# Performance work log

Hardware: AMD Instinct MI355X
Metric: run time of the kernel (lower is better)

## Reference

```python
import jax, jax.numpy as jnp
import numpy as np

DELTA_A, DELTA_R = 0.1, 1.0
ALPHA, BETA, GAMMA = 1.0, 1.0, 0.001


def setup_inputs() -> dict:
    key = jax.random.key(0)
    B, D, H, W, K = 4, 32, 512, 512, 16
    out = jax.random.normal(key, (B, D, H, W), dtype=jnp.float32)
    # 4x4 block partition -> K=16 instance labels, one center per block
    gh, gw = 4, 4
    bh, bw = H // gh, W // gw
    rows = np.arange(H) // bh  # [H]
    cols = np.arange(W) // bw  # [W]
    labels = (rows[:, None] * gw + cols[None, :]).astype(np.int32)  # [H,W]
    target = jnp.asarray(np.broadcast_to(labels, (B, H, W)).copy())
    ctr = np.array([[r * bh + bh // 2, c * bw + bw // 2]
                    for r in range(gh) for c in range(gw)], dtype=np.int32)  # [K,2]
    centers = jnp.asarray(np.broadcast_to(ctr, (B, K, 2)).copy())
    return {"out": out, "target": target, "centers": centers, "batch_size": B}


def _safe_sqrt(x):
    # matches torch.linalg.norm subgradient 0 at 0 (avoids NaN grads)
    pos = x > 0
    return jnp.where(pos, jnp.sqrt(jnp.where(pos, x, 1.0)), 0.0)


def _pairwise_norm(a, b):
    # a [M,D], b [N,D] -> [M,N] euclidean distances via gram trick
    d2 = (jnp.sum(a * a, 1)[:, None] + jnp.sum(b * b, 1)[None, :]
          - 2.0 * a @ b.T)
    return _safe_sqrt(jax.nn.relu(d2))


def _per_image(o, t, c):
    # o [D,H,W], t [H,W] int, c [K,2] int
    D = o.shape[0]
    K = c.shape[0]
    x = o.reshape(D, -1).T                      # [HW, D]
    E = o[:, c[:, 0], c[:, 1]].T                # [K, D] center embeddings
    lab_c = t[c[:, 0], c[:, 1]]                 # [K]
    mask = (t.reshape(-1)[None, :] == lab_c[:, None])  # [K, HW]
    # attraction: hinged distance of every cluster pixel to its center
    norms = _pairwise_norm(E, x)                # [K, HW]
    hinged = jax.nn.relu(norms - DELTA_A) * mask
    cnt = jnp.sum(mask, axis=1)
    denom = jnp.maximum(cnt - 1, 1).astype(o.dtype)
    s_att = jnp.sum(jnp.sum(hinged, axis=1) / denom)
    # repelling: pairwise center distances; diagonal contributes relu(delta_r)
    # per row and the original subtracts delta_r per center -> excluded
    nE = _pairwise_norm(E, E)                   # [K, K]
    s_rep = jnp.sum(jax.nn.relu(DELTA_R - nE)) - K * DELTA_R
    # regularization: norm of each center embedding
    s_reg = jnp.sum(_safe_sqrt(jnp.sum(E * E, axis=1)))
    return s_att, s_rep, s_reg


def reference(out, target, centers, batch_size):
    K = centers.shape[1]
    s_att, s_rep, s_reg = jax.vmap(_per_image)(out, target, centers)  # [B] each
    div_att = jnp.float32(K)
    div_rep = jnp.float32(K * (K - 1))
    div_reg = jnp.float32(K)

    def step(carry, s):
        a, r, g = carry
        sa, sr, sg = s
        return ((a + sa) / div_att, (r + sr) / div_rep, (g + sg) / div_reg), None

    zero = jnp.float32(0.0)
    (att, rep, reg), _ = jax.lax.scan(step, (zero, zero, zero),
                                      (s_att, s_rep, s_reg))
    loss = ALPHA * att + BETA * rep + GAMMA * reg
    return loss, att, rep
```

## Files before the change

### kernel.cpp

```cpp
#include <hip/hip_runtime.h>
#include <hip/hip_bf16.h>

#define B_ 4
#define D_ 32
#define H_ 512
#define W_ 512
#define K_ 16
#define N_ (H_ * W_)
#define NQ_ (N_ / 4)
#define NBLK_ 256
#define EPAD 33

#define WS_SUM  0
#define WS_CNT  64
#define WS_E2   128
#define WS_LAB  192
#define WS_E    264
#define WS_PART 4096

typedef float vfloat4 __attribute__((ext_vector_type(4)));
typedef int vint4 __attribute__((ext_vector_type(4)));

__device__ inline vfloat4 nt_load_f4(const float* p) {
  return __builtin_nontemporal_load((const vfloat4*)p);
}
__device__ inline vint4 nt_load_i4(const int* p) {
  return __builtin_nontemporal_load((const vint4*)p);
}

__global__ __launch_bounds__(64) void setup_kernel(
    const float* __restrict__ outp, const int* __restrict__ target,
    const int* __restrict__ centers, float* __restrict__ ws) {
  const int b = blockIdx.x, k = blockIdx.y;
  const int lane = threadIdx.x;
  const int cy = centers[(b * K_ + k) * 2 + 0];
  const int cx = centers[(b * K_ + k) * 2 + 1];
  float v = 0.0f;
  if (lane < D_) {
    v = outp[(((size_t)b * D_ + lane) * H_ + cy) * W_ + cx];
    ws[WS_E + (b * K_ + k) * D_ + lane] = v;
  }
  float s = v * v;
  for (int off = 32; off > 0; off >>= 1) s += __shfl_xor(s, off, 64);
  if (lane == 0) {
    ws[WS_E2 + b * K_ + k] = s;
    ((int*)ws)[WS_LAB + b * K_ + k] = target[(size_t)b * N_ + cy * W_ + cx];
  }
}

__global__ __launch_bounds__(256) void attract_kernel(
    const float* __restrict__ outp, const int* __restrict__ target,
    float* __restrict__ ws) {
  const int b = blockIdx.y;
  const int tid = threadIdx.x;
  __shared__ float sE[K_ * EPAD];
  __shared__ float se2[K_];
  __shared__ int slab[K_];
  __shared__ float bs[K_];
  __shared__ float bc[K_];

  if (tid < 128) {
    const vfloat4 v = *(const vfloat4*)(ws + WS_E + b * (K_ * D_) + tid * 4);
    const int k = tid >> 3, d = (tid & 7) * 4;
    sE[k * EPAD + d + 0] = v.x;
    sE[k * EPAD + d + 1] = v.y;
    sE[k * EPAD + d + 2] = v.z;
    sE[k * EPAD + d + 3] = v.w;
  }
  if (tid < K_) {
    se2[tid] = ws[WS_E2 + b * K_ + tid];
    slab[tid] = ((const int*)ws)[WS_LAB + b * K_ + tid];
    bs[tid] = 0.0f;
    bc[tid] = 0.0f;
  }
  __syncthreads();

  const int q = blockIdx.x * 256 + tid;
  const float* xb = outp + (size_t)b * D_ * N_;
  const vint4 lab4 = nt_load_i4(target + (size_t)b * N_ + 4 * q);
  const int labv[4] = {lab4.x, lab4.y, lab4.z, lab4.w};

  int kf[4], nm[4];
#pragma unroll
  for (int j = 0; j < 4; ++j) { kf[j] = 0; nm[j] = 0; }
#pragma unroll
  for (int k = 0; k < K_; ++k) {
    const int lk = slab[k];
#pragma unroll
    for (int j = 0; j < 4; ++j) {
      if (labv[j] == lk) { if (nm[j] == 0) kf[j] = k; nm[j]++; }
    }
  }

  float dot[4] = {0.f, 0.f, 0.f, 0.f};
  float x2[4] = {0.f, 0.f, 0.f, 0.f};
#pragma unroll
  for (int d = 0; d < D_; ++d) {
    const vfloat4 x = nt_load_f4(xb + (size_t)d * N_ + 4 * q);
    const float xs[4] = {x.x, x.y, x.z, x.w};
#pragma unroll
    for (int j = 0; j < 4; ++j) {
      const float e = sE[kf[j] * EPAD + d];
      dot[j] = fmaf(xs[j], e, dot[j]);
      x2[j] = fmaf(xs[j], xs[j], x2[j]);
    }
  }

  float hv[4];
#pragma unroll
  for (int j = 0; j < 4; ++j) {
    const float d2 = x2[j] + se2[kf[j]] - 2.0f * dot[j];
    const float h = fmaxf(sqrtf(fmaxf(d2, 0.0f)) - 0.1f, 0.0f);
    hv[j] = (nm[j] > 0) ? h : 0.0f;
  }
  const bool same = (kf[0] == kf[1]) & (kf[1] == kf[2]) & (kf[2] == kf[3]);
  if (same) {
    const float cs = (float)((nm[0] > 0) + (nm[1] > 0) + (nm[2] > 0) + (nm[3] > 0));
    if (cs > 0.0f) {
      atomicAdd(&bs[kf[0]], hv[0] + hv[1] + hv[2] + hv[3]);
      atomicAdd(&bc[kf[0]], cs);
    }
  } else {
#pragma unroll
    for (int j = 0; j < 4; ++j) {
      if (nm[j] > 0) {
        atomicAdd(&bs[kf[j]], hv[j]);
        atomicAdd(&bc[kf[j]], 1.0f);
      }
    }
  }

  const bool extra = (nm[0] > 1) | (nm[1] > 1) | (nm[2] > 1) | (nm[3] > 1);
  if (__any(extra)) {
    for (int k = 0; k < K_; ++k) {
      bool need[4]; bool anyn = false;
#pragma unroll
      for (int j = 0; j < 4; ++j) {
        need[j] = (nm[j] > 1) && (labv[j] == slab[k]) && (k != kf[j]);
        anyn |= need[j];
      }
      if (__any(anyn)) {
        float dt[4] = {0.f, 0.f, 0.f, 0.f};
        for (int d = 0; d < D_; ++d) {
          const vfloat4 x = nt_load_f4(xb + (size_t)d * N_ + 4 * q);
          const float e = sE[k * EPAD + d];
          dt[0] = fmaf(x.x, e, dt[0]);
          dt[1] = fmaf(x.y, e, dt[1]);
          dt[2] = fmaf(x.z, e, dt[2]);
          dt[3] = fmaf(x.w, e, dt[3]);
        }
#pragma unroll
        for (int j = 0; j < 4; ++j) {
          if (need[j]) {
            const float d2 = x2[j] + se2[k] - 2.0f * dt[j];
            atomicAdd(&bs[k], fmaxf(sqrtf(fmaxf(d2, 0.0f)) - 0.1f, 0.0f));
            atomicAdd(&bc[k], 1.0f);
          }
        }
      }
    }
  }
  __syncthreads();

  if (tid < 2 * K_) {
    float* p = ws + WS_PART + ((size_t)b * NBLK_ + blockIdx.x) * (2 * K_);
    p[tid] = (tid < K_) ? bs[tid] : bc[tid - K_];
  }
}

__global__ __launch_bounds__(256) void reduce_kernel(const float* __restrict__ ws_in,
                                                     float* __restrict__ ws) {
  const int b = blockIdx.x >> 4, k = blockIdx.x & 15;
  const int tid = threadIdx.x;
  const float* base = ws_in + WS_PART + (size_t)b * NBLK_ * (2 * K_);
  float s = 0.0f, c = 0.0f;
  for (int i = tid; i < NBLK_; i += 256) {
    s += base[i * (2 * K_) + k];
    c += base[i * (2 * K_) + K_ + k];
  }
  for (int off = 32; off > 0; off >>= 1) {
    s += __shfl_xor(s, off, 64);
    c += __shfl_xor(c, off, 64);
  }
  __shared__ float rs[4], rc[4];
  if ((tid & 63) == 0) { rs[tid >> 6] = s; rc[tid >> 6] = c; }
  __syncthreads();
  if (tid == 0) {
    ws[WS_SUM + b * K_ + k] = rs[0] + rs[1] + rs[2] + rs[3];
    ws[WS_CNT + b * K_ + k] = rc[0] + rc[1] + rc[2] + rc[3];
  }
}

__global__ __launch_bounds__(256) void final_kernel(const float* __restrict__ ws,
                                                    float* __restrict__ out) {
  __shared__ float sE[B_ * K_ * D_];
  __shared__ float sred[256];
  __shared__ float srep[B_];
  __shared__ float sreg[B_];
  __shared__ float ssa[B_];
  const int tid = threadIdx.x;
  for (int i = tid; i < B_ * K_ * D_; i += 256) sE[i] = ws[WS_E + i];
  __syncthreads();

  const int i = tid >> 4, j = tid & 15;
  for (int b = 0; b < B_; ++b) {
    float dotv = 0.0f;
#pragma unroll 8
    for (int d = 0; d < D_; ++d)
      dotv = fmaf(sE[(b * K_ + i) * D_ + d], sE[(b * K_ + j) * D_ + d], dotv);
    const float d2 = ws[WS_E2 + b * K_ + i] + ws[WS_E2 + b * K_ + j] - 2.0f * dotv;
    sred[tid] = fmaxf(1.0f - sqrtf(fmaxf(d2, 0.0f)), 0.0f);
    __syncthreads();
    for (int s = 128; s > 0; s >>= 1) {
      if (tid < s) sred[tid] += sred[tid + s];
      __syncthreads();
    }
    if (tid == 0) srep[b] = sred[0] - (float)K_;
    __syncthreads();
  }

  sred[tid] = (tid < B_ * K_) ? sqrtf(fmaxf(ws[WS_E2 + tid], 0.0f)) : 0.0f;
  __syncthreads();
  if (tid < B_) {
    float s = 0.0f;
    for (int k = 0; k < K_; ++k) s += sred[tid * K_ + k];
    sreg[tid] = s;
  }

  if (tid < B_ * K_) {
    const float c = ws[WS_CNT + tid];
    float v = ws[WS_SUM + tid] / fmaxf(c - 1.0f, 1.0f);
    for (int off = 1; off < K_; off <<= 1) v += __shfl_xor(v, off, 64);
    if ((tid & 15) == 0) ssa[tid >> 4] = v;
  }
  __syncthreads();

  if (tid == 0) {
    float att = 0.0f, rep = 0.0f, reg = 0.0f;
    for (int b = 0; b < B_; ++b) {
      att = (att + ssa[b]) / (float)K_;
      rep = (rep + srep[b]) / (float)(K_ * (K_ - 1));
      reg = (reg + sreg[b]) / (float)K_;
    }
    out[0] = att + rep + 0.001f * reg;
    out[1] = att;
    out[2] = rep;
  }
}

extern "C" void kernel_launch(void* const* d_in, const int* in_sizes, int n_in,
                              void* d_out, int out_size, void* d_ws, size_t ws_size,
                              hipStream_t stream) {
  const float* outp = (const float*)d_in[0];
  const int* target = (const int*)d_in[1];
  const int* centers = (const int*)d_in[2];
  float* ws = (float*)d_ws;
  float* out = (float*)d_out;

  setup_kernel<<<dim3(B_, K_), 64, 0, stream>>>(outp, target, centers, ws);
  attract_kernel<<<dim3(NBLK_, B_), 256, 0, stream>>>(outp, target, ws);
  reduce_kernel<<<dim3(B_ * K_), 256, 0, stream>>>(ws, ws);
  final_kernel<<<1, 256, 0, stream>>>(ws, out);
}
```

Measured before the change: 200.5 us.

## Fuse setup and reduce kernels into attract/final and add wave-level atomic aggregation

Each attract block now gathers the center embeddings, their squared norms and labels itself, which removes the separate setup launch at the cost of redundant center loads per block. The per-block partial reduction moves into the final kernel, so the dedicated reduce launch is gone. A 32-lane shuffle reduction collapses the shared-memory atomics when all lanes map to the same cluster. Together these cut the pipeline from four launches to two and reduce atomic contention.

Result: no change. 201.6 us (+0.6%).

```diff
diff --git a/kernel.cpp b/kernel.cpp
--- a/kernel.cpp
+++ b/kernel.cpp
@@ -1,5 +1,4 @@
 #include <hip/hip_runtime.h>
-#include <hip/hip_bf16.h>
 
 #define B_ 4
 #define D_ 32
@@ -28,50 +27,44 @@
   return __builtin_nontemporal_load((const vint4*)p);
 }
 
-__global__ __launch_bounds__(64) void setup_kernel(
+__global__ __launch_bounds__(256) void attract_kernel(
     const float* __restrict__ outp, const int* __restrict__ target,
     const int* __restrict__ centers, float* __restrict__ ws) {
-  const int b = blockIdx.x, k = blockIdx.y;
-  const int lane = threadIdx.x;
-  const int cy = centers[(b * K_ + k) * 2 + 0];
-  const int cx = centers[(b * K_ + k) * 2 + 1];
-  float v = 0.0f;
-  if (lane < D_) {
-    v = outp[(((size_t)b * D_ + lane) * H_ + cy) * W_ + cx];
-    ws[WS_E + (b * K_ + k) * D_ + lane] = v;
-  }
-  float s = v * v;
-  for (int off = 32; off > 0; off >>= 1) s += __shfl_xor(s, off, 64);
-  if (lane == 0) {
-    ws[WS_E2 + b * K_ + k] = s;
-    ((int*)ws)[WS_LAB + b * K_ + k] = target[(size_t)b * N_ + cy * W_ + cx];
-  }
-}
-
-__global__ __launch_bounds__(256) void attract_kernel(
-    const float* __restrict__ outp, const int* __restrict__ target,
-    float* __restrict__ ws) {
   const int b = blockIdx.y;
   const int tid = threadIdx.x;
   __shared__ float sE[K_ * EPAD];
   __shared__ float se2[K_];
   __shared__ int slab[K_];
+  __shared__ int scy[K_], scx[K_];
   __shared__ float bs[K_];
   __shared__ float bc[K_];
 
-  if (tid < 128) {
-    const vfloat4 v = *(const vfloat4*)(ws + WS_E + b * (K_ * D_) + tid * 4);
-    const int k = tid >> 3, d = (tid & 7) * 4;
-    sE[k * EPAD + d + 0] = v.x;
-    sE[k * EPAD + d + 1] = v.y;
-    sE[k * EPAD + d + 2] = v.z;
-    sE[k * EPAD + d + 3] = v.w;
-  }
-  if (tid < K_) {
-    se2[tid] = ws[WS_E2 + b * K_ + tid];
-    slab[tid] = ((const int*)ws)[WS_LAB + b * K_ + tid];
-    bs[tid] = 0.0f;
-    bc[tid] = 0.0f;
+  if (tid < 2 * K_) {
+    const int v = centers[b * (2 * K_) + tid];
+    if (tid & 1) scx[tid >> 1] = v; else scy[tid >> 1] = v;
+  }
+  __syncthreads();
+  {
+    const int k = tid >> 4, d0 = tid & 15;
+    const size_t cbase = ((size_t)b * D_ * H_ + scy[k]) * W_ + scx[k];
+    const float v0 = outp[cbase + (size_t)d0 * N_];
+    const float v1 = outp[cbase + (size_t)(d0 + 16) * N_];
+    sE[k * EPAD + d0] = v0;
+    sE[k * EPAD + d0 + 16] = v1;
+    float p = fmaf(v0, v0, v1 * v1);
+#pragma unroll
+    for (int off = 1; off < 16; off <<= 1) p += __shfl_xor(p, off, 64);
+    if (blockIdx.x == 0) {
+      ws[WS_E + (b * K_ + k) * D_ + d0] = v0;
+      ws[WS_E + (b * K_ + k) * D_ + d0 + 16] = v1;
+      if ((tid & 15) == 0) ws[WS_E2 + b * K_ + k] = p;
+    }
+    if ((tid & 15) == 0) se2[k] = p;
+    if (tid < K_) {
+      slab[tid] = target[(size_t)b * N_ + scy[tid] * W_ + scx[tid]];
+      bs[tid] = 0.0f;
+      bc[tid] = 0.0f;
+    }
   }
   __syncthreads();
 
@@ -113,12 +106,30 @@
     const float h = fmaxf(sqrtf(fmaxf(d2, 0.0f)) - 0.1f, 0.0f);
     hv[j] = (nm[j] > 0) ? h : 0.0f;
   }
+
   const bool same = (kf[0] == kf[1]) & (kf[1] == kf[2]) & (kf[2] == kf[3]);
-  if (same) {
-    const float cs = (float)((nm[0] > 0) + (nm[1] > 0) + (nm[2] > 0) + (nm[3] > 0));
-    if (cs > 0.0f) {
-      atomicAdd(&bs[kf[0]], hv[0] + hv[1] + hv[2] + hv[3]);
-      atomicAdd(&bc[kf[0]], cs);
+  float hsum = hv[0] + hv[1] + hv[2] + hv[3];
+  float csum = (float)((nm[0] > 0) + (nm[1] > 0) + (nm[2] > 0) + (nm[3] > 0));
+  int gi = same ? (kf[0] + 1) : 0;
+#pragma unroll
+  for (int off = 1; off < 32; off <<= 1) {
+    const int o = __shfl_xor(gi, off, 64);
+    if (o != gi) gi = 0;
+  }
+  if (gi != 0) {
+#pragma unroll
+    for (int off = 1; off < 32; off <<= 1) {
+      hsum += __shfl_xor(hsum, off, 64);
+      csum += __shfl_xor(csum, off, 64);
+    }
+    if ((tid & 31) == 0 && csum > 0.0f) {
+      atomicAdd(&bs[gi - 1], hsum);
+      atomicAdd(&bc[gi - 1], csum);
+    }
+  } else if (same) {
+    if (csum > 0.0f) {
+      atomicAdd(&bs[kf[0]], hsum);
+      atomicAdd(&bc[kf[0]], csum);
     }
   } else {
 #pragma unroll
@@ -168,38 +179,42 @@
   }
 }
 
-__global__ __launch_bounds__(256) void reduce_kernel(const float* __restrict__ ws_in,
-                                                     float* __restrict__ ws) {
-  const int b = blockIdx.x >> 4, k = blockIdx.x & 15;
-  const int tid = threadIdx.x;
-  const float* base = ws_in + WS_PART + (size_t)b * NBLK_ * (2 * K_);
-  float s = 0.0f, c = 0.0f;
-  for (int i = tid; i < NBLK_; i += 256) {
-    s += base[i * (2 * K_) + k];
-    c += base[i * (2 * K_) + K_ + k];
-  }
-  for (int off = 32; off > 0; off >>= 1) {
-    s += __shfl_xor(s, off, 64);
-    c += __shfl_xor(c, off, 64);
-  }
-  __shared__ float rs[4], rc[4];
-  if ((tid & 63) == 0) { rs[tid >> 6] = s; rc[tid >> 6] = c; }
-  __syncthreads();
-  if (tid == 0) {
-    ws[WS_SUM + b * K_ + k] = rs[0] + rs[1] + rs[2] + rs[3];
-    ws[WS_CNT + b * K_ + k] = rc[0] + rc[1] + rc[2] + rc[3];
-  }
-}
-
 __global__ __launch_bounds__(256) void final_kernel(const float* __restrict__ ws,
                                                     float* __restrict__ out) {
+  const int tid = threadIdx.x;
   __shared__ float sE[B_ * K_ * D_];
+  __shared__ float ps[4][64], pc[4][64];
   __shared__ float sred[256];
   __shared__ float srep[B_];
   __shared__ float sreg[B_];
   __shared__ float ssa[B_];
-  const int tid = threadIdx.x;
+
   for (int i = tid; i < B_ * K_ * D_; i += 256) sE[i] = ws[WS_E + i];
+
+  const int pair = tid & 63, quarter = tid >> 6;
+  const int pb = pair >> 4, pk = pair & 15;
+  {
+    const float* base =
+        ws + WS_PART + ((size_t)pb * NBLK_ + quarter * 64) * (2 * K_);
+    float s = 0.0f, c = 0.0f;
+#pragma unroll 4
+    for (int i = 0; i < 64; ++i) {
+      s += base[i * (2 * K_) + pk];
+      c += base[i * (2 * K_) + K_ + pk];
+    }
+    ps[quarter][pair] = s;
+    pc[quarter][pair] = c;
+  }
+  __syncthreads();
+
+  if (tid < 64) {
+    const float s = ps[0][tid] + ps[1][tid] + ps[2][tid] + ps[3][tid];
+    const float c = pc[0][tid] + pc[1][tid] + pc[2][tid] + pc[3][tid];
+    float v = s / fmaxf(c - 1.0f, 1.0f);
+#pragma unroll
+    for (int off = 1; off < K_; off <<= 1) v += __shfl_xor(v, off, 64);
+    if ((tid & 15) == 0) ssa[tid >> 4] = v;
+  }
   __syncthreads();
 
   const int i = tid >> 4, j = tid & 15;
@@ -222,16 +237,9 @@
   sred[tid] = (tid < B_ * K_) ? sqrtf(fmaxf(ws[WS_E2 + tid], 0.0f)) : 0.0f;
   __syncthreads();
   if (tid < B_) {
-    float s = 0.0f;
-    for (int k = 0; k < K_; ++k) s += sred[tid * K_ + k];
-    sreg[tid] = s;
-  }
-
-  if (tid < B_ * K_) {
-    const float c = ws[WS_CNT + tid];
-    float v = ws[WS_SUM + tid] / fmaxf(c - 1.0f, 1.0f);
-    for (int off = 1; off < K_; off <<= 1) v += __shfl_xor(v, off, 64);
-    if ((tid & 15) == 0) ssa[tid >> 4] = v;
+    float sg = 0.0f;
+    for (int k = 0; k < K_; ++k) sg += sred[tid * K_ + k];
+    sreg[tid] = sg;
   }
   __syncthreads();
 
@@ -257,8 +265,6 @@
   float* ws = (float*)d_ws;
   float* out = (float*)d_out;
 
-  setup_kernel<<<dim3(B_, K_), 64, 0, stream>>>(outp, target, centers, ws);
-  attract_kernel<<<dim3(NBLK_, B_), 256, 0, stream>>>(outp, target, ws);
-  reduce_kernel<<<dim3(B_ * K_), 256, 0, stream>>>(ws, ws);
+  attract_kernel<<<dim3(NBLK_, B_), 256, 0, stream>>>(outp, target, centers, ws);
   final_kernel<<<1, 256, 0, stream>>>(ws, out);
 }
```
